# Kernel optimization log

Measured on AMD Instinct MI355X. Metric: run time of the kernel, lower is better.

Reference implementation:

```python
import jax, jax.numpy as jnp
import numpy as np

N = 100_000      # nodes
E = 1_600_000    # edges (avg degree 16)
DIN = 128        # input_dim
DOUT = 64        # output_dim
BJORCK_ITERS = 5


def setup_inputs() -> dict:
    key = jax.random.key(0)
    ks = jax.random.split(key, 4)
    x = jax.random.normal(ks[0], (N, DIN), dtype=jnp.float32)
    edge_index = jax.random.randint(ks[1], (2, E), 0, N)
    ar = jnp.arange(N)
    edge_index_id = jnp.stack([ar, ar])  # self-loop edge list
    # positive degree-like values in [1, 64]
    diags = jax.random.uniform(ks[2], (N,), dtype=jnp.float32) * 63.0 + 1.0
    # GCNConv lin weight [out, in], xavier-uniform-ish scale; bias [out] zeros
    std = float(np.sqrt(2.0 / (DIN + DOUT)))
    W = jax.random.normal(ks[3], (DOUT, DIN), dtype=jnp.float32) * std
    b = jnp.zeros((DOUT,), dtype=jnp.float32)
    one = jnp.ones((1,), jnp.float32)
    zero = jnp.zeros((1,), jnp.float32)
    # SYMLAPLACIAN init: m1=0, m2=-1, m3=1, e1=0, e2=-0.5, e3=-0.5
    return dict(x=x, edge_index=edge_index, edge_index_id=edge_index_id,
                diags=diags, W=W, b=b,
                m1=zero, m2=-one, m3=one,
                e1=zero, e2=-0.5 * one, e3=-0.5 * one)


def _safe_pow(d, e):
    p = jnp.power(d, e)
    return jnp.where(jnp.isinf(p), 0.0, p)


def _bjorck(w, iters=BJORCK_ITERS):
    # spectral-norm rescale then Bjorck-Bowie iterations (shapes are static)
    w = w / (jnp.linalg.norm(w, ord=2) * 1.1)
    for _ in range(iters):
        if w.shape[0] < w.shape[1]:
            w = 1.5 * w - 0.5 * (w @ w.T) @ w
        else:
            w = 1.5 * w - 0.5 * w @ (w.T @ w)
    return w


def reference(x, edge_index, edge_index_id, diags, W, b, m1, m2, m3, e1, e2, e3):
    n = x.shape[0]
    row, col = edge_index[0], edge_index[1]
    row_id, col_id = edge_index_id[0], edge_index_id[1]

    # GSO 1: per-edge weight m2 * d[row]^e2 * d[col]^e3
    d_e2 = _safe_pow(diags, e2)
    d_e3 = _safe_pow(diags, e3)
    gso_1 = m2 * (d_e2[row] * d_e3[col])                         # [E]

    # GSO 2 (self-loop edges): m1*d^e1 + m2*d^e2*d^e3 + m3
    d_e1 = _safe_pow(diags, e1)
    gso_2 = m1 * d_e1[row_id] + m2 * (d_e2[row_id] * d_e3[col_id]) + m3  # [N]

    # GCNConv with explicit edge weights (normalize=False):
    #   out[col] += w_e * (x @ W_orth^T)[row]; then + bias
    Wo = _bjorck(W)
    xw = x @ Wo.T                                                # [N, DOUT]
    h1 = jax.ops.segment_sum(gso_1[:, None] * xw[row], col, num_segments=n) + b
    h2 = jax.ops.segment_sum(gso_2[:, None] * xw[row_id], col_id, num_segments=n) + b
    h = h1 + h2
    # single layer -> no relu/dropout; final log-softmax over classes
    return jax.nn.log_softmax(h, axis=1)
```

## Files before the change

kernel.cpp:

```cpp
#include <hip/hip_runtime.h>
#include <math.h>

#define DIN 128
#define DOUT 64

#define NBLK 64
#define BK_SHIFT 7
#define BK_COLS 128
#define NBK_STRIDE 1024
#define CCAP 4096

__device__ __forceinline__ float safe_pow(float d, float e) {
    float p = powf(d, e);
    return isinf(p) ? 0.0f : p;
}

__device__ __forceinline__ float dot4(float4 a, float4 b) {
    return a.x * b.x + a.y * b.y + a.z * b.z + a.w * b.w;
}

__device__ __forceinline__ unsigned short f32_to_bf16(float f) {
    unsigned bits = __float_as_uint(f);
    unsigned r = (bits + 0x7FFFu + ((bits >> 16) & 1u)) >> 16;
    return (unsigned short)r;
}

__global__ __launch_bounds__(256) void mm_pass(const float* A1, const float* A2,
                                               const float* Bsrc,
                                               float* C1, float* C2, float* CB) {
    int t = threadIdx.x;
    bool second = (blockIdx.x >= 8);
    int blk = blockIdx.x & 7;
    const float* As = second ? A2 : A1;
    float* Cs = second ? C2 : C1;
    int c = t & 63;
    int r0 = blk * 8 + (t >> 6) * 2;
    float acc0 = 0.f, acc1 = 0.f;
#pragma unroll
    for (int k4 = 0; k4 < 16; ++k4) {
        float4 b  = *(const float4*)&Bsrc[c * 64 + k4 * 4];
        float4 a0 = *(const float4*)&As[r0 * 64 + k4 * 4];
        float4 a1 = *(const float4*)&As[(r0 + 1) * 64 + k4 * 4];
        acc0 += dot4(a0, b);
        acc1 += dot4(a1, b);
    }
    Cs[r0 * 64 + c] = acc0;
    Cs[(r0 + 1) * 64 + c] = acc1;
    if (CB != nullptr && !second) {
        CB[r0 * 64 + c]       = ((r0 == c)     ? 1.5f : 0.0f) - 0.5f * acc0;
        CB[(r0 + 1) * 64 + c] = ((r0 + 1 == c) ? 1.5f : 0.0f) - 0.5f * acc1;
    }
}

__global__ __launch_bounds__(256) void gram_pass(const float* W, float* G) {
    int t = threadIdx.x;
    int c = t & 63;
    int r0 = blockIdx.x * 8 + (t >> 6) * 2;
    float acc0 = 0.f, acc1 = 0.f;
#pragma unroll
    for (int k4 = 0; k4 < 32; ++k4) {
        float4 b  = *(const float4*)&W[c * 128 + k4 * 4];
        float4 a0 = *(const float4*)&W[r0 * 128 + k4 * 4];
        float4 a1 = *(const float4*)&W[(r0 + 1) * 128 + k4 * 4];
        acc0 += dot4(a0, b);
        acc1 += dot4(a1, b);
    }
    G[r0 * 64 + c] = acc0;
    G[(r0 + 1) * 64 + c] = acc1;
}

__global__ __launch_bounds__(64) void power_pass(const float* gH2, float* gSc) {
    int t = threadIdx.x;
    float tr = gH2[t * 65];
#pragma unroll
    for (int d = 1; d < 64; d <<= 1) tr += __shfl_xor(tr, d);
    float inv_tr = 1.0f / tr;
    float4 g4[16];
#pragma unroll
    for (int j4 = 0; j4 < 16; ++j4) {
        float4 v = *(const float4*)&gH2[t * 64 + j4 * 4];
        v.x *= inv_tr; v.y *= inv_tr; v.z *= inv_tr; v.w *= inv_tr;
        g4[j4] = v;
    }
    unsigned h = (unsigned)t * 2654435761u;
    float xv = 0.5f + (float)((h >> 17) & 0x7fff) * (1.0f / 32768.0f);
    float yv = 0.f;
    for (int it = 0; it < 8; ++it) {
        float p0 = 0.f, p1 = 0.f, p2 = 0.f, p3 = 0.f;
#pragma unroll
        for (int j4 = 0; j4 < 16; ++j4) {
            float4 xx;
            xx.x = __shfl(xv, j4 * 4 + 0);
            xx.y = __shfl(xv, j4 * 4 + 1);
            xx.z = __shfl(xv, j4 * 4 + 2);
            xx.w = __shfl(xv, j4 * 4 + 3);
            float dd = dot4(g4[j4], xx);
            if (j4 < 4) p0 += dd; else if (j4 < 8) p1 += dd;
            else if (j4 < 12) p2 += dd; else p3 += dd;
        }
        yv = (p0 + p1) + (p2 + p3);
        if (it < 7) xv = yv;
    }
    float num = xv * yv, den = xv * xv;
#pragma unroll
    for (int d = 1; d < 64; d <<= 1) {
        num += __shfl_xor(num, d);
        den += __shfl_xor(den, d);
    }
    if (t == 0) {
        float lam_h2 = tr * num / den;
        float sig = powf(lam_h2, 0.125f);
        gSc[0] = 1.0f / (1.1f * sig);
        gSc[1] = 1.0f / (1.21f * sig * sig);
    }
}

__global__ __launch_bounds__(256) void prep_pass(const float* gG, const float* gSc,
                                                 float* gA0, float* gB0) {
    int idx = blockIdx.x * 256 + threadIdx.x;
    if (idx >= 4096) return;
    float rs = gSc[1];
    int r = idx >> 6, c = idx & 63;
    float a0 = rs * gG[idx];
    gA0[idx] = a0;
    gB0[idx] = ((r == c) ? 1.5f : 0.0f) - 0.5f * a0;
}

__global__ __launch_bounds__(256) void wo_pass(const float* W, const float* P,
                                               const float* gSc, float* Wo) {
    int t = threadIdx.x;
    int c = t & 63;
    int r0 = blockIdx.x * 8 + (t >> 6) * 2;
    float a00 = 0.f, a01 = 0.f, a10 = 0.f, a11 = 0.f;
#pragma unroll 4
    for (int j = 0; j < 64; ++j) {
        float p0 = P[r0 * 64 + j];
        float p1 = P[(r0 + 1) * 64 + j];
        float w0 = W[j * 128 + c];
        float w1 = W[j * 128 + c + 64];
        a00 += p0 * w0; a01 += p0 * w1;
        a10 += p1 * w0; a11 += p1 * w1;
    }
    float sc = gSc[0];
    Wo[r0 * 128 + c]            = sc * a00;
    Wo[r0 * 128 + c + 64]       = sc * a01;
    Wo[(r0 + 1) * 128 + c]      = sc * a10;
    Wo[(r0 + 1) * 128 + c + 64] = sc * a11;
}

__global__ void node_prep(const float* __restrict__ diags,
                          const float* m1, const float* m2, const float* m3,
                          const float* e1, const float* e2, const float* e3,
                          float* __restrict__ d_e2m, float* __restrict__ d_e3p,
                          float* __restrict__ gso2, int n) {
    int i = blockIdx.x * blockDim.x + threadIdx.x;
    if (i >= n) return;
    float d = diags[i];
    float p1 = safe_pow(d, e1[0]);
    float p2 = safe_pow(d, e2[0]);
    float p3 = safe_pow(d, e3[0]);
    float vm2 = m2[0];
    d_e2m[i] = vm2 * p2;
    d_e3p[i] = p3;
    gso2[i] = m1[0] * p1 + vm2 * p2 * p3 + m3[0];
}

#define XN 64
#define XS 132
__global__ __launch_bounds__(256) void xw_kernel(const float* __restrict__ x,
                                                 const float* __restrict__ Wo,
                                                 unsigned short* __restrict__ xwb,
                                                 int n) {
    __shared__ __align__(16) float xs[XN * XS];
    __shared__ __align__(16) float ws[DOUT * XS];
    int t = threadIdx.x;
    int base = blockIdx.x * XN;
    for (int f = t; f < DOUT * (DIN / 4); f += 256) {
        int r = f >> 5, c = f & 31;
        *(float4*)&ws[r * XS + c * 4] = *(const float4*)&Wo[r * DIN + c * 4];
    }
    for (int f = t; f < XN * (DIN / 4); f += 256) {
        int r = f >> 5, c = f & 31;
        int node = base + r;
        float4 v = make_float4(0.f, 0.f, 0.f, 0.f);
        if (node < n) v = *(const float4*)&x[(size_t)node * DIN + c * 4];
        *(float4*)&xs[r * XS + c * 4] = v;
    }
    __syncthreads();
    int tn = t >> 4;
    int td = t & 15;
    float acc[4][4] = {};
#pragma unroll 2
    for (int k4 = 0; k4 < DIN / 4; ++k4) {
        float4 a[4], w[4];
#pragma unroll
        for (int r = 0; r < 4; ++r) a[r] = *(const float4*)&xs[(tn * 4 + r) * XS + k4 * 4];
#pragma unroll
        for (int c = 0; c < 4; ++c) w[c] = *(const float4*)&ws[(td + c * 16) * XS + k4 * 4];
#pragma unroll
        for (int r = 0; r < 4; ++r)
#pragma unroll
            for (int c = 0; c < 4; ++c) acc[r][c] += dot4(a[r], w[c]);
    }
#pragma unroll
    for (int r = 0; r < 4; ++r) {
        int node = base + tn * 4 + r;
        if (node >= n) break;
#pragma unroll
        for (int c = 0; c < 4; ++c)
            xwb[(size_t)node * DOUT + td + c * 16] = f32_to_bf16(acc[r][c]);
    }
}

__global__ __launch_bounds__(256) void b1_hist(const int* __restrict__ ei,
                                               unsigned* __restrict__ blk_hist,
                                               int e_cnt, int chunk, int nbk) {
    __shared__ int h[NBK_STRIDE];
    int b = blockIdx.x, t = threadIdx.x;
    for (int j = t; j < NBK_STRIDE; j += 256) h[j] = 0;
    __syncthreads();
    int lo = b * chunk, hi = min(lo + chunk, e_cnt);
    for (int e = lo + t; e < hi; e += 256)
        atomicAdd(&h[ei[e_cnt + e] >> BK_SHIFT], 1);
    __syncthreads();
    for (int j = t; j < nbk; j += 256)
        blk_hist[(size_t)b * NBK_STRIDE + j] = (unsigned)h[j];
}

__global__ __launch_bounds__(1024) void s_scan(unsigned* __restrict__ blk_hist,
                                               unsigned* __restrict__ bucket_offsets,
                                               int nbk, int e_cnt) {
    __shared__ int tot[1024];
    int t = threadIdx.x;
    int total = 0;
    if (t < nbk) {
        int run = 0;
        for (int b = 0; b < NBLK; ++b) {
            size_t idx = (size_t)b * NBK_STRIDE + t;
            int v = (int)blk_hist[idx];
            blk_hist[idx] = (unsigned)run;
            run += v;
        }
        total = run;
    }
    tot[t] = total;
    __syncthreads();
    for (int d = 1; d < 1024; d <<= 1) {
        int u = (t >= d) ? tot[t - d] : 0;
        __syncthreads();
        tot[t] += u;
        __syncthreads();
    }
    int excl = tot[t] - total;
    if (t < nbk) {
        bucket_offsets[t] = (unsigned)excl;
        for (int b = 0; b < NBLK; ++b)
            blk_hist[(size_t)b * NBK_STRIDE + t] += (unsigned)excl;
    }
    if (t == 0) bucket_offsets[nbk] = (unsigned)e_cnt;
}

__global__ __launch_bounds__(256) void b2_scatter(const int* __restrict__ ei,
                                                  const unsigned* __restrict__ blk_hist,
                                                  unsigned* __restrict__ bucketed,
                                                  int e_cnt, int chunk, int nbk) {
    __shared__ int cur[NBK_STRIDE];
    int b = blockIdx.x, t = threadIdx.x;
    for (int j = t; j < nbk; j += 256)
        cur[j] = (int)blk_hist[(size_t)b * NBK_STRIDE + j];
    __syncthreads();
    int lo = b * chunk, hi = min(lo + chunk, e_cnt);
    for (int e = lo + t; e < hi; e += 256) {
        int col = ei[e_cnt + e];
        int src = ei[e];
        int bkt = col >> BK_SHIFT;
        int pos = atomicAdd(&cur[bkt], 1);
        bucketed[pos] = ((unsigned)src << BK_SHIFT) | (unsigned)(col & (BK_COLS - 1));
    }
}

__global__ __launch_bounds__(256) void c_csr(const unsigned* __restrict__ bucketed,
                                             const unsigned* __restrict__ bucket_offsets,
                                             const float* __restrict__ d_e2m,
                                             int* __restrict__ offsets,
                                             uint2* __restrict__ pairs,
                                             int n, int e_cnt) {
    __shared__ unsigned sE[CCAP];
    __shared__ int sh[BK_COLS];
    __shared__ int sc[BK_COLS];
    __shared__ int pos_[BK_COLS];
    int b = blockIdx.x, t = threadIdx.x;
    int base = (int)bucket_offsets[b];
    int cnt = (int)bucket_offsets[b + 1] - base;
    bool fits = (cnt <= CCAP);
    if (fits)
        for (int i = t; i < cnt; i += 256) sE[i] = bucketed[base + i];
    if (t < BK_COLS) sh[t] = 0;
    __syncthreads();
    for (int i = t; i < cnt; i += 256) {
        unsigned p = fits ? sE[i] : bucketed[base + i];
        atomicAdd(&sh[p & (BK_COLS - 1)], 1);
    }
    __syncthreads();
    if (t < BK_COLS) sc[t] = sh[t];
    __syncthreads();
    for (int d = 1; d < BK_COLS; d <<= 1) {
        int u = 0;
        if (t < BK_COLS && t >= d) u = sc[t - d];
        __syncthreads();
        if (t < BK_COLS) sc[t] += u;
        __syncthreads();
    }
    if (t < BK_COLS) {
        int pre = sc[t] - sh[t];
        int gc = b * BK_COLS + t;
        if (gc < n) offsets[gc] = base + pre;
        pos_[t] = pre;
    }
    if (b == 0 && t == 0) offsets[n] = e_cnt;
    __syncthreads();
    for (int i = t; i < cnt; i += 256) {
        unsigned p = fits ? sE[i] : bucketed[base + i];
        int lc = (int)(p & (BK_COLS - 1));
        unsigned s = p >> BK_SHIFT;
        int q = atomicAdd(&pos_[lc], 1);
        uint2 o;
        o.x = s;
        o.y = __float_as_uint(d_e2m[s]);
        pairs[base + q] = o;
    }
}

__global__ __launch_bounds__(256) void gather_kernel(const int* __restrict__ offsets,
                                                     const uint2* __restrict__ pairs,
                                                     const float* __restrict__ d_e3p,
                                                     const unsigned short* __restrict__ xwb,
                                                     const float* __restrict__ gso2,
                                                     const float* __restrict__ b,
                                                     float* __restrict__ out, int n) {
    unsigned lane = threadIdx.x & 63;
    unsigned half = lane >> 5;
    unsigned hl = lane & 31;
    int node = blockIdx.x * 4 + (threadIdx.x >> 6);
    if (node >= n) return;
    int lo = offsets[node], hi = offsets[node + 1];
    const unsigned* xw32 = (const unsigned*)xwb;
    float accLo = 0.f, accHi = 0.f;
    int i = lo;
    for (; i + 8 <= hi; i += 8) {
        int e0 = i + 4 * half;
        uint2 p0 = pairs[e0 + 0], p1 = pairs[e0 + 1];
        uint2 p2 = pairs[e0 + 2], p3 = pairs[e0 + 3];
        unsigned u0 = xw32[p0.x * 32u + hl];
        unsigned u1 = xw32[p1.x * 32u + hl];
        unsigned u2 = xw32[p2.x * 32u + hl];
        unsigned u3 = xw32[p3.x * 32u + hl];
        float w0 = __uint_as_float(p0.y), w1 = __uint_as_float(p1.y);
        float w2 = __uint_as_float(p2.y), w3 = __uint_as_float(p3.y);
        accLo += w0 * __uint_as_float(u0 << 16) + w1 * __uint_as_float(u1 << 16)
               + w2 * __uint_as_float(u2 << 16) + w3 * __uint_as_float(u3 << 16);
        accHi += w0 * __uint_as_float(u0 & 0xFFFF0000u) + w1 * __uint_as_float(u1 & 0xFFFF0000u)
               + w2 * __uint_as_float(u2 & 0xFFFF0000u) + w3 * __uint_as_float(u3 & 0xFFFF0000u);
    }
    for (; i + 4 <= hi; i += 4) {
        int e0 = i + 2 * half;
        uint2 p0 = pairs[e0 + 0], p1 = pairs[e0 + 1];
        unsigned u0 = xw32[p0.x * 32u + hl];
        unsigned u1 = xw32[p1.x * 32u + hl];
        float w0 = __uint_as_float(p0.y), w1 = __uint_as_float(p1.y);
        accLo += w0 * __uint_as_float(u0 << 16) + w1 * __uint_as_float(u1 << 16);
        accHi += w0 * __uint_as_float(u0 & 0xFFFF0000u) + w1 * __uint_as_float(u1 & 0xFFFF0000u);
    }
    {
        int rem = hi - i;
        int j0 = 2 * (int)half;
        int j1 = min(j0 + 2, rem);
        for (int j = j0; j < j1; ++j) {
            uint2 p = pairs[i + j];
            unsigned u = xw32[p.x * 32u + hl];
            float w = __uint_as_float(p.y);
            accLo += w * __uint_as_float(u << 16);
            accHi += w * __uint_as_float(u & 0xFFFF0000u);
        }
    }
    accLo += __shfl_xor(accLo, 32);
    accHi += __shfl_xor(accHi, 32);

    unsigned us = xw32[(unsigned)node * 32u + hl];
    float xsLo = __uint_as_float(us << 16);
    float xsHi = __uint_as_float(us & 0xFFFF0000u);
    float2 bb = *(const float2*)&b[2 * hl];
    float gs = gso2[node], dn = d_e3p[node];
    float vLo = gs * xsLo + 2.0f * bb.x + dn * accLo;
    float vHi = gs * xsHi + 2.0f * bb.y + dn * accHi;
    float m = fmaxf(vLo, vHi);
#pragma unroll
    for (int d = 1; d < 32; d <<= 1) m = fmaxf(m, __shfl_xor(m, d));
    float s = expf(vLo - m) + expf(vHi - m);
#pragma unroll
    for (int d = 1; d < 32; d <<= 1) s += __shfl_xor(s, d);
    if (half == 0) {
        float ls = logf(s);
        float2 o;
        o.x = vLo - m - ls;
        o.y = vHi - m - ls;
        *(float2*)&out[(size_t)node * DOUT + 2 * hl] = o;
    }
}

extern "C" void kernel_launch(void* const* d_in, const int* in_sizes, int n_in,
                              void* d_out, int out_size, void* d_ws, size_t ws_size,
                              hipStream_t stream) {
    const float* x     = (const float*)d_in[0];
    const int*   ei    = (const int*)d_in[1];
    const float* diags = (const float*)d_in[3];
    const float* W     = (const float*)d_in[4];
    const float* b     = (const float*)d_in[5];
    const float* m1    = (const float*)d_in[6];
    const float* m2    = (const float*)d_in[7];
    const float* m3    = (const float*)d_in[8];
    const float* e1    = (const float*)d_in[9];
    const float* e2    = (const float*)d_in[10];
    const float* e3    = (const float*)d_in[11];
    float* out = (float*)d_out;

    const int n = in_sizes[3];
    const int e_cnt = in_sizes[1] / 2;
    const int nbk = (n + BK_COLS - 1) >> BK_SHIFT;
    const int chunk = (e_cnt + NBLK - 1) / NBLK;

    char* ws = (char*)d_ws;
    float*    Wo   = (float*)ws;
    float*    gG   = (float*)(ws + 32768);
    float*    gT   = gG  + 4096;
    float*    gA   = gT  + 4096;
    float*    gAn  = gA  + 4096;
    float*    gA0  = gAn + 4096;
    float*    gP   = gA0 + 4096;
    float*    gPn  = gP  + 4096;
    float*    gB0  = gPn + 4096;
    float*    gB1  = gB0 + 4096;
    float*    gB2  = gB1 + 4096;
    float*    gB3  = gB2 + 4096;
    float*    gB4  = gB3 + 4096;
    float*    gSc  = gB4 + 4096;
    float*          d_e2m    = gSc + 64;
    float*          d_e3p    = d_e2m + n;
    float*          gso2     = d_e3p + n;
    unsigned short* xwb      = (unsigned short*)(gso2 + n);
    int*            offsets  = (int*)(xwb + (size_t)n * DOUT);
    unsigned*       bucketed = (unsigned*)(offsets + n + 4);
    unsigned*       blk_hist = bucketed + e_cnt;
    unsigned*       boff     = blk_hist + (size_t)NBLK * NBK_STRIDE;
    uintptr_t pp = ((uintptr_t)(boff + nbk + 8) + 15) & ~(uintptr_t)15;
    uint2*          pairs    = (uint2*)pp;

    gram_pass<<<8, 256, 0, stream>>>(W, gG);
    mm_pass<<<8, 256, 0, stream>>>(gG, nullptr, gG, gT, nullptr, nullptr);
    mm_pass<<<8, 256, 0, stream>>>(gT, nullptr, gT, gA, nullptr, nullptr);
    power_pass<<<1, 64, 0, stream>>>(gA, gSc);
    prep_pass<<<16, 256, 0, stream>>>(gG, gSc, gA0, gB0);
    mm_pass<<<8, 256, 0, stream>>>(gA0, nullptr, gB0, gT, nullptr, nullptr);
    mm_pass<<<8, 256, 0, stream>>>(gT, nullptr, gB0, gA, nullptr, gB1);
    mm_pass<<<16, 256, 0, stream>>>(gB0, gA, gB1, gP, gT, nullptr);
    mm_pass<<<8, 256, 0, stream>>>(gT, nullptr, gB1, gAn, nullptr, gB2);
    mm_pass<<<16, 256, 0, stream>>>(gP, gAn, gB2, gPn, gT, nullptr);
    mm_pass<<<8, 256, 0, stream>>>(gT, nullptr, gB2, gA, nullptr, gB3);
    mm_pass<<<16, 256, 0, stream>>>(gPn, gA, gB3, gP, gT, nullptr);
    mm_pass<<<8, 256, 0, stream>>>(gT, nullptr, gB3, gAn, nullptr, gB4);
    mm_pass<<<8, 256, 0, stream>>>(gP, nullptr, gB4, gPn, nullptr, nullptr);
    wo_pass<<<8, 256, 0, stream>>>(W, gPn, gSc, Wo);

    node_prep<<<(n + 255) / 256, 256, 0, stream>>>(diags, m1, m2, m3, e1, e2, e3,
                                                   d_e2m, d_e3p, gso2, n);
    xw_kernel<<<(n + XN - 1) / XN, 256, 0, stream>>>(x, Wo, xwb, n);
    b1_hist<<<NBLK, 256, 0, stream>>>(ei, blk_hist, e_cnt, chunk, nbk);
    s_scan<<<1, 1024, 0, stream>>>(blk_hist, boff, nbk, e_cnt);
    b2_scatter<<<NBLK, 256, 0, stream>>>(ei, blk_hist, bucketed, e_cnt, chunk, nbk);
    c_csr<<<nbk, 256, 0, stream>>>(bucketed, boff, d_e2m, offsets, pairs, n, e_cnt);
    gather_kernel<<<(n + 3) / 4, 256, 0, stream>>>(offsets, pairs, d_e3p,
                                                   xwb, gso2, b, out, n);
}
```

Baseline: 259.2 us.

## Fuse CSR build with neighbor gather and merge power/prep kernels

Merges the per-bucket CSR construction and the per-node gather/log-softmax into one kernel. Each 512-thread block sorts its 128-column bucket into shared memory as (src, weight) pairs and then gathers directly from LDS, which removes the global pairs array round trip and the offsets array. Buckets larger than the shared capacity spill to global memory. It also fuses the power-iteration and prep kernels into a single launch. In exchange there are fewer blocks (one per 128 nodes), only 8 waves per block for gather latency hiding, and larger LDS use per block.

Measured after the change: 254.8 us. No clear change (-1.7%).

```diff
diff --git a/kernel.cpp b/kernel.cpp
--- a/kernel.cpp
+++ b/kernel.cpp
@@ -8,7 +8,7 @@
 #define BK_SHIFT 7
 #define BK_COLS 128
 #define NBK_STRIDE 1024
-#define CCAP 4096
+#define CCAP 3072
 
 __device__ __forceinline__ float safe_pow(float d, float e) {
     float p = powf(d, e);
@@ -69,61 +69,64 @@
     G[(r0 + 1) * 64 + c] = acc1;
 }
 
-__global__ __launch_bounds__(64) void power_pass(const float* gH2, float* gSc) {
-    int t = threadIdx.x;
-    float tr = gH2[t * 65];
-#pragma unroll
-    for (int d = 1; d < 64; d <<= 1) tr += __shfl_xor(tr, d);
-    float inv_tr = 1.0f / tr;
-    float4 g4[16];
-#pragma unroll
-    for (int j4 = 0; j4 < 16; ++j4) {
-        float4 v = *(const float4*)&gH2[t * 64 + j4 * 4];
-        v.x *= inv_tr; v.y *= inv_tr; v.z *= inv_tr; v.w *= inv_tr;
-        g4[j4] = v;
-    }
-    unsigned h = (unsigned)t * 2654435761u;
-    float xv = 0.5f + (float)((h >> 17) & 0x7fff) * (1.0f / 32768.0f);
-    float yv = 0.f;
-    for (int it = 0; it < 8; ++it) {
-        float p0 = 0.f, p1 = 0.f, p2 = 0.f, p3 = 0.f;
+__global__ __launch_bounds__(256) void power_prep(const float* gH2, const float* gG,
+                                                  float* gSc, float* gA0, float* gB0) {
+    __shared__ float sS[2];
+    int t = threadIdx.x;
+    if (t < 64) {
+        float tr = gH2[t * 65];
+#pragma unroll
+        for (int d = 1; d < 64; d <<= 1) tr += __shfl_xor(tr, d);
+        float inv_tr = 1.0f / tr;
+        float4 g4[16];
 #pragma unroll
         for (int j4 = 0; j4 < 16; ++j4) {
-            float4 xx;
-            xx.x = __shfl(xv, j4 * 4 + 0);
-            xx.y = __shfl(xv, j4 * 4 + 1);
-            xx.z = __shfl(xv, j4 * 4 + 2);
-            xx.w = __shfl(xv, j4 * 4 + 3);
-            float dd = dot4(g4[j4], xx);
-            if (j4 < 4) p0 += dd; else if (j4 < 8) p1 += dd;
-            else if (j4 < 12) p2 += dd; else p3 += dd;
-        }
-        yv = (p0 + p1) + (p2 + p3);
-        if (it < 7) xv = yv;
-    }
-    float num = xv * yv, den = xv * xv;
-#pragma unroll
-    for (int d = 1; d < 64; d <<= 1) {
-        num += __shfl_xor(num, d);
-        den += __shfl_xor(den, d);
-    }
-    if (t == 0) {
-        float lam_h2 = tr * num / den;
-        float sig = powf(lam_h2, 0.125f);
-        gSc[0] = 1.0f / (1.1f * sig);
-        gSc[1] = 1.0f / (1.21f * sig * sig);
-    }
-}
-
-__global__ __launch_bounds__(256) void prep_pass(const float* gG, const float* gSc,
-                                                 float* gA0, float* gB0) {
-    int idx = blockIdx.x * 256 + threadIdx.x;
-    if (idx >= 4096) return;
-    float rs = gSc[1];
-    int r = idx >> 6, c = idx & 63;
-    float a0 = rs * gG[idx];
-    gA0[idx] = a0;
-    gB0[idx] = ((r == c) ? 1.5f : 0.0f) - 0.5f * a0;
+            float4 v = *(const float4*)&gH2[t * 64 + j4 * 4];
+            v.x *= inv_tr; v.y *= inv_tr; v.z *= inv_tr; v.w *= inv_tr;
+            g4[j4] = v;
+        }
+        unsigned h = (unsigned)t * 2654435761u;
+        float xv = 0.5f + (float)((h >> 17) & 0x7fff) * (1.0f / 32768.0f);
+        float yv = 0.f;
+        for (int it = 0; it < 8; ++it) {
+            float p0 = 0.f, p1 = 0.f, p2 = 0.f, p3 = 0.f;
+#pragma unroll
+            for (int j4 = 0; j4 < 16; ++j4) {
+                float4 xx;
+                xx.x = __shfl(xv, j4 * 4 + 0);
+                xx.y = __shfl(xv, j4 * 4 + 1);
+                xx.z = __shfl(xv, j4 * 4 + 2);
+                xx.w = __shfl(xv, j4 * 4 + 3);
+                float dd = dot4(g4[j4], xx);
+                if (j4 < 4) p0 += dd; else if (j4 < 8) p1 += dd;
+                else if (j4 < 12) p2 += dd; else p3 += dd;
+            }
+            yv = (p0 + p1) + (p2 + p3);
+            if (it < 7) xv = yv;
+        }
+        float num = xv * yv, den = xv * xv;
+#pragma unroll
+        for (int d = 1; d < 64; d <<= 1) {
+            num += __shfl_xor(num, d);
+            den += __shfl_xor(den, d);
+        }
+        if (t == 0) {
+            float lam_h2 = tr * num / den;
+            float sig = powf(lam_h2, 0.125f);
+            float sc = 1.0f / (1.1f * sig);
+            float rs = 1.0f / (1.21f * sig * sig);
+            gSc[0] = sc; gSc[1] = rs;
+            sS[0] = sc; sS[1] = rs;
+        }
+    }
+    __syncthreads();
+    float rs = sS[1];
+    for (int idx = t; idx < 4096; idx += 256) {
+        int r = idx >> 6, c2 = idx & 63;
+        float a0 = rs * gG[idx];
+        gA0[idx] = a0;
+        gB0[idx] = ((r == c2) ? 1.5f : 0.0f) - 0.5f * a0;
+    }
 }
 
 __global__ __launch_bounds__(256) void wo_pass(const float* W, const float* P,
@@ -279,132 +282,130 @@
     }
 }
 
-__global__ __launch_bounds__(256) void c_csr(const unsigned* __restrict__ bucketed,
-                                             const unsigned* __restrict__ bucket_offsets,
-                                             const float* __restrict__ d_e2m,
-                                             int* __restrict__ offsets,
-                                             uint2* __restrict__ pairs,
-                                             int n, int e_cnt) {
-    __shared__ unsigned sE[CCAP];
-    __shared__ int sh[BK_COLS];
-    __shared__ int sc[BK_COLS];
-    __shared__ int pos_[BK_COLS];
+__global__ __launch_bounds__(512) void csr_gather(const unsigned* __restrict__ bucketed,
+                                                  const unsigned* __restrict__ boff,
+                                                  const float* __restrict__ d_e2m,
+                                                  const float* __restrict__ d_e3p,
+                                                  const unsigned short* __restrict__ xwb,
+                                                  const float* __restrict__ gso2,
+                                                  const float* __restrict__ bias,
+                                                  uint2* __restrict__ spill,
+                                                  float* __restrict__ out, int n) {
+    __shared__ __align__(16) uint2 sP[CCAP];
+    __shared__ int shc[BK_COLS], scc[BK_COLS], posc[BK_COLS];
+    __shared__ int offs[BK_COLS + 1];
     int b = blockIdx.x, t = threadIdx.x;
-    int base = (int)bucket_offsets[b];
-    int cnt = (int)bucket_offsets[b + 1] - base;
+    int base = (int)boff[b];
+    int cnt = (int)boff[b + 1] - base;
     bool fits = (cnt <= CCAP);
-    if (fits)
-        for (int i = t; i < cnt; i += 256) sE[i] = bucketed[base + i];
-    if (t < BK_COLS) sh[t] = 0;
-    __syncthreads();
-    for (int i = t; i < cnt; i += 256) {
-        unsigned p = fits ? sE[i] : bucketed[base + i];
-        atomicAdd(&sh[p & (BK_COLS - 1)], 1);
-    }
-    __syncthreads();
-    if (t < BK_COLS) sc[t] = sh[t];
+
+    if (t < BK_COLS) shc[t] = 0;
+    __syncthreads();
+    for (int i = t; i < cnt; i += 512)
+        atomicAdd(&shc[bucketed[base + i] & (BK_COLS - 1)], 1);
+    __syncthreads();
+    if (t < BK_COLS) scc[t] = shc[t];
     __syncthreads();
     for (int d = 1; d < BK_COLS; d <<= 1) {
         int u = 0;
-        if (t < BK_COLS && t >= d) u = sc[t - d];
+        if (t < BK_COLS && t >= d) u = scc[t - d];
         __syncthreads();
-        if (t < BK_COLS) sc[t] += u;
+        if (t < BK_COLS) scc[t] += u;
         __syncthreads();
     }
     if (t < BK_COLS) {
-        int pre = sc[t] - sh[t];
-        int gc = b * BK_COLS + t;
-        if (gc < n) offsets[gc] = base + pre;
-        pos_[t] = pre;
-    }
-    if (b == 0 && t == 0) offsets[n] = e_cnt;
-    __syncthreads();
-    for (int i = t; i < cnt; i += 256) {
-        unsigned p = fits ? sE[i] : bucketed[base + i];
-        int lc = (int)(p & (BK_COLS - 1));
-        unsigned s = p >> BK_SHIFT;
-        int q = atomicAdd(&pos_[lc], 1);
-        uint2 o;
-        o.x = s;
-        o.y = __float_as_uint(d_e2m[s]);
-        pairs[base + q] = o;
-    }
-}
-
-__global__ __launch_bounds__(256) void gather_kernel(const int* __restrict__ offsets,
-                                                     const uint2* __restrict__ pairs,
-                                                     const float* __restrict__ d_e3p,
-                                                     const unsigned short* __restrict__ xwb,
-                                                     const float* __restrict__ gso2,
-                                                     const float* __restrict__ b,
-                                                     float* __restrict__ out, int n) {
-    unsigned lane = threadIdx.x & 63;
+        int pre = scc[t] - shc[t];
+        posc[t] = pre;
+        offs[t] = pre;
+    }
+    if (t == 0) offs[BK_COLS] = cnt;
+    __syncthreads();
+    {
+        uint2* dst = fits ? (uint2*)sP : (spill + base);
+        for (int i = t; i < cnt; i += 512) {
+            unsigned k = bucketed[base + i];
+            unsigned lc = k & (BK_COLS - 1);
+            unsigned src = k >> BK_SHIFT;
+            int q = atomicAdd(&posc[lc], 1);
+            uint2 o;
+            o.x = src;
+            o.y = __float_as_uint(d_e2m[src]);
+            dst[q] = o;
+        }
+    }
+    __syncthreads();
+
+    const uint2* P = fits ? (const uint2*)sP : (const uint2*)(spill + base);
+    unsigned lane = t & 63;
     unsigned half = lane >> 5;
     unsigned hl = lane & 31;
-    int node = blockIdx.x * 4 + (threadIdx.x >> 6);
-    if (node >= n) return;
-    int lo = offsets[node], hi = offsets[node + 1];
+    int wv = t >> 6;
     const unsigned* xw32 = (const unsigned*)xwb;
-    float accLo = 0.f, accHi = 0.f;
-    int i = lo;
-    for (; i + 8 <= hi; i += 8) {
-        int e0 = i + 4 * half;
-        uint2 p0 = pairs[e0 + 0], p1 = pairs[e0 + 1];
-        uint2 p2 = pairs[e0 + 2], p3 = pairs[e0 + 3];
-        unsigned u0 = xw32[p0.x * 32u + hl];
-        unsigned u1 = xw32[p1.x * 32u + hl];
-        unsigned u2 = xw32[p2.x * 32u + hl];
-        unsigned u3 = xw32[p3.x * 32u + hl];
-        float w0 = __uint_as_float(p0.y), w1 = __uint_as_float(p1.y);
-        float w2 = __uint_as_float(p2.y), w3 = __uint_as_float(p3.y);
-        accLo += w0 * __uint_as_float(u0 << 16) + w1 * __uint_as_float(u1 << 16)
-               + w2 * __uint_as_float(u2 << 16) + w3 * __uint_as_float(u3 << 16);
-        accHi += w0 * __uint_as_float(u0 & 0xFFFF0000u) + w1 * __uint_as_float(u1 & 0xFFFF0000u)
-               + w2 * __uint_as_float(u2 & 0xFFFF0000u) + w3 * __uint_as_float(u3 & 0xFFFF0000u);
-    }
-    for (; i + 4 <= hi; i += 4) {
-        int e0 = i + 2 * half;
-        uint2 p0 = pairs[e0 + 0], p1 = pairs[e0 + 1];
-        unsigned u0 = xw32[p0.x * 32u + hl];
-        unsigned u1 = xw32[p1.x * 32u + hl];
-        float w0 = __uint_as_float(p0.y), w1 = __uint_as_float(p1.y);
-        accLo += w0 * __uint_as_float(u0 << 16) + w1 * __uint_as_float(u1 << 16);
-        accHi += w0 * __uint_as_float(u0 & 0xFFFF0000u) + w1 * __uint_as_float(u1 & 0xFFFF0000u);
-    }
-    {
-        int rem = hi - i;
-        int j0 = 2 * (int)half;
-        int j1 = min(j0 + 2, rem);
-        for (int j = j0; j < j1; ++j) {
-            uint2 p = pairs[i + j];
-            unsigned u = xw32[p.x * 32u + hl];
-            float w = __uint_as_float(p.y);
-            accLo += w * __uint_as_float(u << 16);
-            accHi += w * __uint_as_float(u & 0xFFFF0000u);
-        }
-    }
-    accLo += __shfl_xor(accLo, 32);
-    accHi += __shfl_xor(accHi, 32);
-
-    unsigned us = xw32[(unsigned)node * 32u + hl];
-    float xsLo = __uint_as_float(us << 16);
-    float xsHi = __uint_as_float(us & 0xFFFF0000u);
-    float2 bb = *(const float2*)&b[2 * hl];
-    float gs = gso2[node], dn = d_e3p[node];
-    float vLo = gs * xsLo + 2.0f * bb.x + dn * accLo;
-    float vHi = gs * xsHi + 2.0f * bb.y + dn * accHi;
-    float m = fmaxf(vLo, vHi);
-#pragma unroll
-    for (int d = 1; d < 32; d <<= 1) m = fmaxf(m, __shfl_xor(m, d));
-    float s = expf(vLo - m) + expf(vHi - m);
-#pragma unroll
-    for (int d = 1; d < 32; d <<= 1) s += __shfl_xor(s, d);
-    if (half == 0) {
-        float ls = logf(s);
-        float2 o;
-        o.x = vLo - m - ls;
-        o.y = vHi - m - ls;
-        *(float2*)&out[(size_t)node * DOUT + 2 * hl] = o;
+    int c0 = wv * 16;
+    for (int c = c0; c < c0 + 16; ++c) {
+        int node = b * BK_COLS + c;
+        if (node >= n) break;
+        int lo = offs[c], hi = offs[c + 1];
+        float accLo = 0.f, accHi = 0.f;
+        int i = lo;
+        for (; i + 8 <= hi; i += 8) {
+            int e0 = i + 4 * (int)half;
+            uint2 p0 = P[e0 + 0], p1 = P[e0 + 1], p2 = P[e0 + 2], p3 = P[e0 + 3];
+            unsigned u0 = xw32[p0.x * 32u + hl];
+            unsigned u1 = xw32[p1.x * 32u + hl];
+            unsigned u2 = xw32[p2.x * 32u + hl];
+            unsigned u3 = xw32[p3.x * 32u + hl];
+            float w0 = __uint_as_float(p0.y), w1 = __uint_as_float(p1.y);
+            float w2 = __uint_as_float(p2.y), w3 = __uint_as_float(p3.y);
+            accLo += w0 * __uint_as_float(u0 << 16) + w1 * __uint_as_float(u1 << 16)
+                   + w2 * __uint_as_float(u2 << 16) + w3 * __uint_as_float(u3 << 16);
+            accHi += w0 * __uint_as_float(u0 & 0xFFFF0000u) + w1 * __uint_as_float(u1 & 0xFFFF0000u)
+                   + w2 * __uint_as_float(u2 & 0xFFFF0000u) + w3 * __uint_as_float(u3 & 0xFFFF0000u);
+        }
+        for (; i + 4 <= hi; i += 4) {
+            int e0 = i + 2 * (int)half;
+            uint2 p0 = P[e0 + 0], p1 = P[e0 + 1];
+            unsigned u0 = xw32[p0.x * 32u + hl];
+            unsigned u1 = xw32[p1.x * 32u + hl];
+            float w0 = __uint_as_float(p0.y), w1 = __uint_as_float(p1.y);
+            accLo += w0 * __uint_as_float(u0 << 16) + w1 * __uint_as_float(u1 << 16);
+            accHi += w0 * __uint_as_float(u0 & 0xFFFF0000u) + w1 * __uint_as_float(u1 & 0xFFFF0000u);
+        }
+        {
+            int rem = hi - i;
+            int j0 = 2 * (int)half;
+            int j1 = min(j0 + 2, rem);
+            for (int j = j0; j < j1; ++j) {
+                uint2 p = P[i + j];
+                unsigned u = xw32[p.x * 32u + hl];
+                float w = __uint_as_float(p.y);
+                accLo += w * __uint_as_float(u << 16);
+                accHi += w * __uint_as_float(u & 0xFFFF0000u);
+            }
+        }
+        accLo += __shfl_xor(accLo, 32);
+        accHi += __shfl_xor(accHi, 32);
+
+        unsigned us = xw32[(unsigned)node * 32u + hl];
+        float xsLo = __uint_as_float(us << 16);
+        float xsHi = __uint_as_float(us & 0xFFFF0000u);
+        float2 bb = *(const float2*)&bias[2 * hl];
+        float gs = gso2[node], dn = d_e3p[node];
+        float vLo = gs * xsLo + 2.0f * bb.x + dn * accLo;
+        float vHi = gs * xsHi + 2.0f * bb.y + dn * accHi;
+        float m = fmaxf(vLo, vHi);
+#pragma unroll
+        for (int d = 1; d < 32; d <<= 1) m = fmaxf(m, __shfl_xor(m, d));
+        float s = expf(vLo - m) + expf(vHi - m);
+#pragma unroll
+        for (int d = 1; d < 32; d <<= 1) s += __shfl_xor(s, d);
+        if (half == 0) {
+            float ls = logf(s);
+            float2 o;
+            o.x = vLo - m - ls;
+            o.y = vHi - m - ls;
+            *(float2*)&out[(size_t)node * DOUT + 2 * hl] = o;
+        }
     }
 }
 
@@ -448,18 +449,16 @@
     float*          d_e3p    = d_e2m + n;
     float*          gso2     = d_e3p + n;
     unsigned short* xwb      = (unsigned short*)(gso2 + n);
-    int*            offsets  = (int*)(xwb + (size_t)n * DOUT);
-    unsigned*       bucketed = (unsigned*)(offsets + n + 4);
+    unsigned*       bucketed = (unsigned*)(xwb + (size_t)n * DOUT);
     unsigned*       blk_hist = bucketed + e_cnt;
     unsigned*       boff     = blk_hist + (size_t)NBLK * NBK_STRIDE;
     uintptr_t pp = ((uintptr_t)(boff + nbk + 8) + 15) & ~(uintptr_t)15;
-    uint2*          pairs    = (uint2*)pp;
+    uint2*          spill    = (uint2*)pp;
 
     gram_pass<<<8, 256, 0, stream>>>(W, gG);
     mm_pass<<<8, 256, 0, stream>>>(gG, nullptr, gG, gT, nullptr, nullptr);
     mm_pass<<<8, 256, 0, stream>>>(gT, nullptr, gT, gA, nullptr, nullptr);
-    power_pass<<<1, 64, 0, stream>>>(gA, gSc);
-    prep_pass<<<16, 256, 0, stream>>>(gG, gSc, gA0, gB0);
+    power_prep<<<1, 256, 0, stream>>>(gA, gG, gSc, gA0, gB0);
     mm_pass<<<8, 256, 0, stream>>>(gA0, nullptr, gB0, gT, nullptr, nullptr);
     mm_pass<<<8, 256, 0, stream>>>(gT, nullptr, gB0, gA, nullptr, gB1);
     mm_pass<<<16, 256, 0, stream>>>(gB0, gA, gB1, gP, gT, nullptr);
@@ -477,7 +476,6 @@
     b1_hist<<<NBLK, 256, 0, stream>>>(ei, blk_hist, e_cnt, chunk, nbk);
     s_scan<<<1, 1024, 0, stream>>>(blk_hist, boff, nbk, e_cnt);
     b2_scatter<<<NBLK, 256, 0, stream>>>(ei, blk_hist, bucketed, e_cnt, chunk, nbk);
-    c_csr<<<nbk, 256, 0, stream>>>(bucketed, boff, d_e2m, offsets, pairs, n, e_cnt);
-    gather_kernel<<<(n + 3) / 4, 256, 0, stream>>>(offsets, pairs, d_e3p,
-                                                   xwb, gso2, b, out, n);
-}
+    csr_gather<<<nbk, 512, 0, stream>>>(bucketed, boff, d_e2m, d_e3p,
+                                        xwb, gso2, b, spill, out, n);
+}
```
